# Kernel tuning notes

Measured on AMD Instinct MI355X. Metric: run time of the kernel, lower is better.

Reference implementation:

```python
import jax, jax.numpy as jnp
import numpy as np

N_NODES = 100000
N_EDGES = 1600000
N_CLASS = 26
HIDDEN = 128


def gcn_conv(x, W, b, row, col, ew, n):
    """PyG GCNConv with normalize=True, add_self_loops=True (fill 1.0).

    row/col/ew already include self-loops. x: [N, Fin], W: [Fin, Fout].
    """
    deg = jax.ops.segment_sum(ew, col, num_segments=n)            # [N]
    dis = jnp.where(deg > 0, jax.lax.rsqrt(jnp.maximum(deg, 1e-30)), 0.0)
    norm = dis[row] * ew * dis[col]                               # [E+N]
    h = x @ W                                                     # [N, Fout]
    msg = h[row] * norm[:, None]                                  # gather + scale
    out = jax.ops.segment_sum(msg, col, num_segments=n)           # scatter-add
    return out + b


def setup_inputs() -> dict:
    key = jax.random.key(0)
    k1, k2, k3, k4, k5, k6, k7, k8, k9 = jax.random.split(key, 9)
    x = jax.random.normal(k1, (N_NODES, N_CLASS), dtype=jnp.float32)
    edge_index = jax.random.randint(k2, (2, N_EDGES), 0, N_NODES, dtype=jnp.int64)
    edge_weight = jax.random.uniform(k3, (N_EDGES,), dtype=jnp.float32)
    s1 = 1.0 / np.sqrt(N_CLASS)
    s2 = 1.0 / np.sqrt(HIDDEN)
    W1 = jax.random.uniform(k4, (N_CLASS, HIDDEN), jnp.float32, -s1, s1)
    b1 = jnp.zeros((HIDDEN,), jnp.float32)
    W2 = jax.random.uniform(k5, (HIDDEN, HIDDEN), jnp.float32, -s2, s2)
    b2 = jnp.zeros((HIDDEN,), jnp.float32)
    Wfc = jax.random.uniform(k6, (HIDDEN, N_CLASS), jnp.float32, -s2, s2)
    bfc = jax.random.uniform(k7, (N_CLASS,), jnp.float32, -s2, s2)
    return {"x": x, "edge_index": edge_index, "edge_weight": edge_weight,
            "W1": W1, "b1": b1, "W2": W2, "b2": b2, "Wfc": Wfc, "bfc": bfc}


def reference(x, edge_index, edge_weight, W1, b1, W2, b2, Wfc, bfc):
    n = x.shape[0]
    loop = jnp.arange(n, dtype=edge_index.dtype)
    row = jnp.concatenate([edge_index[0], loop])   # sources (with self-loops)
    col = jnp.concatenate([edge_index[1], loop])   # targets
    ew = jnp.concatenate([edge_weight, jnp.ones((n,), edge_weight.dtype)])
    h = jax.nn.relu(gcn_conv(x, W1, b1, row, col, ew, n))
    h = jax.nn.relu(gcn_conv(h, W2, b2, row, col, ew, n))
    return h @ Wfc + bfc
```

## Files before the change

kernel.cpp:

```cpp
#include <hip/hip_runtime.h>
#include <hip/hip_fp16.h>

#define N_NODES 100000
#define N_EDGES 1600000
#define HIDDEN  128
#define N_CLASS 26

#define BUK_SHIFT 9
#define BUK_DSTS  512
#define NBUK      196
#define BUK_CAP   10240
#define PB_EDGES  8192
#define PB_BLOCKS ((N_EDGES + PB_EDGES - 1) / PB_EDGES)

typedef _Float16 f16x2 __attribute__((ext_vector_type(2)));

__device__ __forceinline__ float fdot2(__half2 a, __half2 b, float c) {
#if __has_builtin(__builtin_amdgcn_fdot2)
    union { __half2 h; f16x2 v; } ua, ub;
    ua.h = a; ub.h = b;
    return __builtin_amdgcn_fdot2(ua.v, ub.v, c, false);
#else
    float2 fa = __half22float2(a), fb = __half22float2(b);
    return c + fa.x * fb.x + fa.y * fb.y;
#endif
}

union U4 { uint4 u; __half2 h[4]; };
union U2 { uint2 u; __half2 h[2]; };
union UW { int i; __half2 h; };


__global__ __launch_bounds__(1024) void bucket_kernel(const int* __restrict__ row,
                                                      const int* __restrict__ col,
                                                      const float* __restrict__ ew,
                                                      int* __restrict__ bukcnt,
                                                      int2* __restrict__ stage) {
    __shared__ int2 outst[PB_EDGES];
    __shared__ unsigned short bukof[PB_EDGES];
    __shared__ int cnt[NBUK], ofs[NBUK], cur[NBUK], gt[NBUK];
    __shared__ int sc[256];
    const int tid = threadIdx.x;
    const int e0 = blockIdx.x * PB_EDGES;
    const int nvalid = min(PB_EDGES, N_EDGES - e0);

    for (int b = tid; b < NBUK; b += 1024) { cnt[b] = 0; cur[b] = 0; }
    __syncthreads();

    int mykey[8]; float myw[8]; int mybuk[8];
#pragma unroll
    for (int i = 0; i < 8; ++i) {
        int idx = tid + i * 1024;
        mybuk[i] = -1;
        if (idx < nvalid) {
            int e = e0 + idx;
            int d = col[e], r = row[e];
            int buk = d >> BUK_SHIFT;
            mykey[i] = ((d & (BUK_DSTS - 1)) << 17) | r;
            myw[i] = ew[e];
            mybuk[i] = buk;
            atomicAdd(&cnt[buk], 1);
        }
    }
    __syncthreads();

    {
        int c = (tid < NBUK) ? cnt[tid] : 0;
        if (tid < 256) sc[tid] = c;
        __syncthreads();
        for (int o = 1; o < 256; o <<= 1) {
            int v = 0;
            if (tid < 256 && tid >= o) v = sc[tid - o];
            __syncthreads();
            if (tid < 256) sc[tid] += v;
            __syncthreads();
        }
        if (tid < NBUK) ofs[tid] = sc[tid] - c;
        __syncthreads();
    }

#pragma unroll
    for (int i = 0; i < 8; ++i) {
        if (mybuk[i] >= 0) {
            int s = ofs[mybuk[i]] + atomicAdd(&cur[mybuk[i]], 1);
            outst[s] = make_int2(mykey[i], __float_as_int(myw[i]));
            bukof[s] = (unsigned short)mybuk[i];
        }
    }
    __syncthreads();

    if (tid < NBUK) {
        int c = cnt[tid];
        int gb = (c > 0) ? atomicAdd(&bukcnt[tid], c) : 0;
        gt[tid] = tid * BUK_CAP + gb;
    }
    __syncthreads();

    for (int i = tid; i < nvalid; i += 1024) {
        int b = bukof[i];
        stage[(size_t)gt[b] + (i - ofs[b])] = outst[i];
    }
}


__global__ void bukscan_kernel(const int* __restrict__ bukcnt, int* __restrict__ bukbase,
                               int* __restrict__ start) {
    __shared__ int s[256];
    int tid = threadIdx.x;
    int c = (tid < NBUK) ? bukcnt[tid] : 0;
    s[tid] = c;
    __syncthreads();
    for (int o = 1; o < 256; o <<= 1) {
        int v = (tid >= o) ? s[tid - o] : 0;
        __syncthreads();
        s[tid] += v;
        __syncthreads();
    }
    if (tid < NBUK) bukbase[tid] = s[tid] - c;
    if (tid == 0) start[N_NODES] = N_EDGES;
}


__global__ __launch_bounds__(1024) void csr_kernel(const int2* __restrict__ stage,
                                                   const int* __restrict__ bukcnt,
                                                   const int* __restrict__ bukbase,
                                                   const float* __restrict__ x,
                                                   int* __restrict__ start,
                                                   float* __restrict__ dinv,
                                                   __half* __restrict__ x16,
                                                   int2* __restrict__ packed,
                                                   int* __restrict__ perm) {
    __shared__ unsigned int cnt5[BUK_DSTS];
    __shared__ int ofs5[BUK_DSTS];
    __shared__ unsigned int cur5[BUK_DSTS];
    __shared__ float deg5[BUK_DSTS];
    __shared__ float dv5[BUK_DSTS];
    __shared__ int sc[BUK_DSTS];
    __shared__ int dhist[128];
    __shared__ int dcur[128];
    const int tid = threadIdx.x;
    const int b = blockIdx.x;
    const int total = bukcnt[b];
    const int base = bukbase[b];
    const int2* st = stage + (size_t)b * BUK_CAP;

    for (int j = tid; j < BUK_DSTS; j += 1024) { cnt5[j] = 0; cur5[j] = 0; deg5[j] = 0.0f; }
    if (tid < 128) { dhist[tid] = 0; dcur[tid] = 0; }
    __syncthreads();

    for (int i = tid; i < total; i += 1024) {
        int2 en = st[i];
        int dl = en.x >> 17;
        atomicAdd(&cnt5[dl], 1u);
        atomicAdd(&deg5[dl], __int_as_float(en.y));
    }
    __syncthreads();

    {
        int c = (tid < BUK_DSTS) ? (int)cnt5[tid] : 0;
        if (tid < BUK_DSTS) sc[tid] = c;
        __syncthreads();
        for (int o = 1; o < BUK_DSTS; o <<= 1) {
            int v = 0;
            if (tid < BUK_DSTS && tid >= o) v = sc[tid - o];
            __syncthreads();
            if (tid < BUK_DSTS) sc[tid] += v;
            __syncthreads();
        }
        if (tid < BUK_DSTS) ofs5[tid] = sc[tid] - c;
        __syncthreads();
    }

    int myd = -1;
    {
        int d = (b << BUK_SHIFT) + tid;
        if (tid < BUK_DSTS && d < N_NODES) {
            myd = min((int)cnt5[tid], 127);
            atomicAdd(&dhist[myd], 1);
        }
    }

    if (tid < BUK_DSTS) {
        int d = (b << BUK_SHIFT) + tid;
        if (d < N_NODES) {
            float dv = rsqrtf(deg5[tid] + 1.0f);
            dv5[tid] = dv;
            dinv[d] = dv;
            start[d] = base + ofs5[tid];
        }
    }
    __syncthreads();

    if (tid < 128) sc[tid] = dhist[tid];
    __syncthreads();
    for (int o = 1; o < 128; o <<= 1) {
        int v = 0;
        if (tid < 128 && tid >= o) v = sc[tid - o];
        __syncthreads();
        if (tid < 128) sc[tid] += v;
        __syncthreads();
    }
    if (myd >= 0) {
        int rank = sc[myd] - dhist[myd] + atomicAdd(&dcur[myd], 1);
        perm[(b << BUK_SHIFT) + rank] = (b << BUK_SHIFT) + tid;
    }

    for (int t = tid; t < BUK_DSTS * 32; t += 1024) {
        int j = t >> 5, l = t & 31;
        int d = (b << BUK_SHIFT) + j;
        if (d < N_NODES) {
            float v = (l < N_CLASS) ? x[(size_t)d * N_CLASS + l] * dv5[j] : 0.0f;
            x16[((size_t)d << 5) + l] = __float2half(v);
        }
    }

    for (int i = tid; i < total; i += 1024) {
        int2 en = st[i];
        int dl = en.x >> 17;
        int src = en.x & 0x1FFFF;
        unsigned int r = atomicAdd(&cur5[dl], 1u);
        unsigned int hw = __half_as_ushort(__float2half(__int_as_float(en.y)));
        packed[(size_t)base + ofs5[dl] + (int)r] = make_int2(src, (int)(hw | (hw << 16)));
    }
}


__global__ __launch_bounds__(256) void layer1_kernel(const __half* __restrict__ x16,
                                                     const int* __restrict__ start,
                                                     const int2* __restrict__ packed,
                                                     const float* __restrict__ dinv,
                                                     const int* __restrict__ perm,
                                                     const float* __restrict__ W1,
                                                     const float* __restrict__ b1,
                                                     __half* __restrict__ h16) {
    __shared__ float axs[32][32];
    __shared__ int gl[32];
    const int tid = threadIdx.x;
    const int nb = blockIdx.x * 32;
    {
        const int j = tid >> 3;
        const int l = tid & 7;
        const int g = perm[nb + j];
        if (l == 0) gl[j] = g;
        const uint2* X = reinterpret_cast<const uint2*>(x16);
        U2 sv; sv.u = X[((size_t)g << 3) + l];
        __half2 acc0 = sv.h[0], acc1 = sv.h[1];
        int s = start[g], t = start[g + 1];
        int i = s;
        for (; i + 8 <= t; i += 8) {
            int2 pk[8]; U2 vv[8];
#pragma unroll
            for (int u = 0; u < 8; ++u) pk[u] = packed[i + u];
#pragma unroll
            for (int u = 0; u < 8; ++u) vv[u].u = X[((size_t)pk[u].x << 3) + l];
#pragma unroll
            for (int u = 0; u < 8; ++u) {
                UW w; w.i = pk[u].y;
                acc0 = __hfma2(w.h, vv[u].h[0], acc0);
                acc1 = __hfma2(w.h, vv[u].h[1], acc1);
            }
        }
        for (; i < t; ++i) {
            int2 p = packed[i];
            U2 v; v.u = X[((size_t)p.x << 3) + l];
            UW w; w.i = p.y;
            acc0 = __hfma2(w.h, v.h[0], acc0); acc1 = __hfma2(w.h, v.h[1], acc1);
        }
        float dg = dinv[g];
        float2 a = __half22float2(acc0), bb = __half22float2(acc1);
        *reinterpret_cast<float4*>(&axs[j][l * 4]) =
            make_float4(dg * a.x, dg * a.y, dg * bb.x, dg * bb.y);
    }
    __syncthreads();
    const int c = tid & 127;
    const int half = tid >> 7;
    float w[N_CLASS];
#pragma unroll
    for (int k = 0; k < N_CLASS; ++k) w[k] = W1[k * HIDDEN + c];
    const float bias = b1[c];
#pragma unroll
    for (int tt = 0; tt < 16; ++tt) {
        int n = half + 2 * tt;
        float acc = bias;
#pragma unroll
        for (int k = 0; k < N_CLASS; ++k) acc += axs[n][k] * w[k];
        h16[(size_t)gl[n] * HIDDEN + c] = __float2half(fmaxf(acc, 0.0f));
    }
}


#define CB_NODES 128
__global__ __launch_bounds__(512) void gemmC_kernel(const __half* __restrict__ h16,
                                                    const float* __restrict__ W2,
                                                    const float* __restrict__ dinv,
                                                    __half* __restrict__ p16) {
    __shared__ __half2 hs2[CB_NODES][HIDDEN / 2];
    __shared__ __half2 ws2[HIDDEN / 2][HIDDEN];
    const int tid = threadIdx.x;
    const int nb = blockIdx.x * CB_NODES;
    for (int t = tid; t < HIDDEN / 2 * HIDDEN; t += 512) {
        int k2 = t >> 7, c = t & 127;
        ws2[k2][c] = __floats2half2_rn(W2[(2 * k2) * HIDDEN + c], W2[(2 * k2 + 1) * HIDDEN + c]);
    }
    for (int t = tid; t < CB_NODES * 16; t += 512) {
        int node = nb + (t >> 4);
        reinterpret_cast<uint4*>(hs2)[t] =
            (node < N_NODES)
                ? reinterpret_cast<const uint4*>(h16)[(size_t)node * 16 + (t & 15)]
                : make_uint4(0u, 0u, 0u, 0u);
    }
    __syncthreads();
    const int c4 = (tid & 31) * 4;
    const int n0 = (tid >> 5) * 8;
    float acc[8][4] = {};
    for (int k2 = 0; k2 < HIDDEN / 2; k2 += 2) {
        U4 wa, wb;
        wa.u = *reinterpret_cast<const uint4*>(&ws2[k2][c4]);
        wb.u = *reinterpret_cast<const uint4*>(&ws2[k2 + 1][c4]);
#pragma unroll
        for (int i = 0; i < 8; ++i) {
            U2 hv; hv.u = *reinterpret_cast<const uint2*>(&hs2[n0 + i][k2]);
#pragma unroll
            for (int q = 0; q < 4; ++q) {
                acc[i][q] = fdot2(hv.h[0], wa.h[q], acc[i][q]);
                acc[i][q] = fdot2(hv.h[1], wb.h[q], acc[i][q]);
            }
        }
    }
#pragma unroll
    for (int i = 0; i < 8; ++i) {
        int node = nb + n0 + i;
        if (node < N_NODES) {
            float d = dinv[node];
            union { __half2 h2[2]; uint2 u; } pk;
            pk.h2[0] = __floats2half2_rn(d * acc[i][0], d * acc[i][1]);
            pk.h2[1] = __floats2half2_rn(d * acc[i][2], d * acc[i][3]);
            *reinterpret_cast<uint2*>(&p16[(size_t)node * HIDDEN + c4]) = pk.u;
        }
    }
}


__global__ __launch_bounds__(256) void agg2_kernel(const __half* __restrict__ p16,
                                                   const int* __restrict__ start,
                                                   const int2* __restrict__ packed,
                                                   const float* __restrict__ dinv,
                                                   const int* __restrict__ perm,
                                                   const float* __restrict__ b2,
                                                   __half* __restrict__ z16) {
    const int grp = threadIdx.x >> 4;
    const int l   = threadIdx.x & 15;
    const int g   = perm[blockIdx.x * 16 + grp];
    const uint4* P = reinterpret_cast<const uint4*>(p16);

    U4 sv; sv.u = P[((size_t)g << 4) + l];
    __half2 acc0 = sv.h[0], acc1 = sv.h[1], acc2 = sv.h[2], acc3 = sv.h[3];

    int s = start[g], t = start[g + 1];
    int i = s;
    for (; i + 8 <= t; i += 8) {
        int2 pk[8]; U4 vv[8];
#pragma unroll
        for (int u = 0; u < 8; ++u) pk[u] = packed[i + u];
#pragma unroll
        for (int u = 0; u < 8; ++u) vv[u].u = P[((size_t)pk[u].x << 4) + l];
#pragma unroll
        for (int u = 0; u < 8; ++u) {
            UW w; w.i = pk[u].y;
            acc0 = __hfma2(w.h, vv[u].h[0], acc0);
            acc1 = __hfma2(w.h, vv[u].h[1], acc1);
            acc2 = __hfma2(w.h, vv[u].h[2], acc2);
            acc3 = __hfma2(w.h, vv[u].h[3], acc3);
        }
    }
    for (; i + 4 <= t; i += 4) {
        int2 pk[4]; U4 vv[4];
#pragma unroll
        for (int u = 0; u < 4; ++u) pk[u] = packed[i + u];
#pragma unroll
        for (int u = 0; u < 4; ++u) vv[u].u = P[((size_t)pk[u].x << 4) + l];
#pragma unroll
        for (int u = 0; u < 4; ++u) {
            UW w; w.i = pk[u].y;
            acc0 = __hfma2(w.h, vv[u].h[0], acc0);
            acc1 = __hfma2(w.h, vv[u].h[1], acc1);
            acc2 = __hfma2(w.h, vv[u].h[2], acc2);
            acc3 = __hfma2(w.h, vv[u].h[3], acc3);
        }
    }
    for (; i < t; ++i) {
        int2 p = packed[i];
        U4 v; v.u = P[((size_t)p.x << 4) + l];
        UW w; w.i = p.y;
        acc0 = __hfma2(w.h, v.h[0], acc0); acc1 = __hfma2(w.h, v.h[1], acc1);
        acc2 = __hfma2(w.h, v.h[2], acc2); acc3 = __hfma2(w.h, v.h[3], acc3);
    }

    const float dg = dinv[g];
    const int f = l * 8;
    float4 ba = *reinterpret_cast<const float4*>(&b2[f]);
    float4 bb = *reinterpret_cast<const float4*>(&b2[f + 4]);
    float2 f0 = __half22float2(acc0), f1 = __half22float2(acc1);
    float2 f2 = __half22float2(acc2), f3 = __half22float2(acc3);
    U4 zz;
    zz.h[0] = __floats2half2_rn(fmaxf(dg * f0.x + ba.x, 0.f), fmaxf(dg * f0.y + ba.y, 0.f));
    zz.h[1] = __floats2half2_rn(fmaxf(dg * f1.x + ba.z, 0.f), fmaxf(dg * f1.y + ba.w, 0.f));
    zz.h[2] = __floats2half2_rn(fmaxf(dg * f2.x + bb.x, 0.f), fmaxf(dg * f2.y + bb.y, 0.f));
    zz.h[3] = __floats2half2_rn(fmaxf(dg * f3.x + bb.z, 0.f), fmaxf(dg * f3.y + bb.w, 0.f));
    reinterpret_cast<uint4*>(z16)[((size_t)g << 4) + l] = zz.u;
}


#define FC_NODES 128
__global__ __launch_bounds__(256) void fc_kernel(const __half* __restrict__ z16,
                                                 const float* __restrict__ Wfc,
                                                 const float* __restrict__ bfc,
                                                 float* __restrict__ out) {
    __shared__ __align__(16) __half2 zsh[FC_NODES][68];
    const int tid = threadIdx.x;
    const int nb = blockIdx.x * FC_NODES;
    for (int t = tid; t < FC_NODES * 16; t += 256) {
        int n = t >> 4, q = t & 15;
        int node = nb + n;
        uint4 v = (node < N_NODES)
                      ? reinterpret_cast<const uint4*>(z16)[(size_t)node * 16 + q]
                      : make_uint4(0u, 0u, 0u, 0u);
        *reinterpret_cast<uint4*>(&zsh[n][q * 4]) = v;
    }
    const int j = tid & 31;
    const int slice = tid >> 5;
    __half2 wreg[HIDDEN / 2];
    float bj = 0.0f;
    if (j < N_CLASS) {
        bj = bfc[j];
#pragma unroll
        for (int k2 = 0; k2 < HIDDEN / 2; ++k2)
            wreg[k2] = __floats2half2_rn(Wfc[(2 * k2) * N_CLASS + j],
                                         Wfc[(2 * k2 + 1) * N_CLASS + j]);
    }
    __syncthreads();
    if (j >= N_CLASS) return;
    for (int n = slice; n < FC_NODES; n += 8) {
        int node = nb + n;
        if (node < N_NODES) {
            float acc = bj;
#pragma unroll
            for (int k2 = 0; k2 < HIDDEN / 2; ++k2)
                acc = fdot2(zsh[n][k2], wreg[k2], acc);
            out[(size_t)node * N_CLASS + j] = acc;
        }
    }
}


extern "C" void kernel_launch(void* const* d_in, const int* in_sizes, int n_in,
                              void* d_out, int out_size, void* d_ws, size_t ws_size,
                              hipStream_t stream) {
    const float* x   = (const float*)d_in[0];
    const int*   ei  = (const int*)  d_in[1];
    const float* ew  = (const float*)d_in[2];
    const float* W1  = (const float*)d_in[3];
    const float* b1  = (const float*)d_in[4];
    const float* W2  = (const float*)d_in[5];
    const float* b2  = (const float*)d_in[6];
    const float* Wfc = (const float*)d_in[7];
    const float* bfc = (const float*)d_in[8];
    float* out = (float*)d_out;

    const int n = N_NODES, E = N_EDGES;
    const int* row = ei;
    const int* col = ei + E;

    char* ws = (char*)d_ws;
    size_t off = 0;
    auto alloc = [&](size_t bytes) -> void* {
        void* ptr = ws + off;
        off += (bytes + 255) & ~(size_t)255;
        return ptr;
    };
    int*   bukcnt  = (int*)  alloc(NBUK * 4);
    int*   bukbase = (int*)  alloc(NBUK * 4);
    float* dinv    = (float*)alloc((size_t)n * 4);
    int*   start   = (int*)  alloc((size_t)(n + 1) * 4);
    int*   perm    = (int*)  alloc((size_t)n * 4);
    int2*  packed  = (int2*) alloc((size_t)E * 8);
    __half* x16    = (__half*)alloc((size_t)n * 32 * 2);
    __half* h16    = (__half*)alloc((size_t)n * HIDDEN * 2 < (size_t)NBUK * BUK_CAP * 8
                                        ? (size_t)NBUK * BUK_CAP * 8
                                        : (size_t)n * HIDDEN * 2);
    __half* p16    = (__half*)alloc((size_t)n * HIDDEN * 2);
    int2*  stage   = (int2*)h16;
    __half* z16    = h16;

    hipMemsetAsync(bukcnt, 0, NBUK * 4, stream);
    bucket_kernel<<<PB_BLOCKS, 1024, 0, stream>>>(row, col, ew, bukcnt, stage);
    bukscan_kernel<<<1, 256, 0, stream>>>(bukcnt, bukbase, start);
    csr_kernel<<<NBUK, 1024, 0, stream>>>(stage, bukcnt, bukbase, x, start, dinv, x16, packed, perm);

    layer1_kernel<<<(n + 31) / 32, 256, 0, stream>>>(x16, start, packed, dinv, perm, W1, b1, h16);

    gemmC_kernel<<<(n + CB_NODES - 1) / CB_NODES, 512, 0, stream>>>(h16, W2, dinv, p16);
    agg2_kernel<<<(n + 15) / 16, 256, 0, stream>>>(p16, start, packed, dinv, perm, b2, z16);

    fc_kernel<<<(n + FC_NODES - 1) / FC_NODES, 256, 0, stream>>>(z16, Wfc, bfc, out);
}
```

Measured before the change: 237.0 us.

## Fuse final linear layer into layer-2 aggregation and use smaller destination buckets

The second-layer aggregation kernel now applies bias and ReLU, stages each node's hidden vector in shared memory, and computes the 26-class output directly from it. This removes the separate fc kernel and the fp16 intermediate write and re-read. Bucketing is also changed to 256 destinations per bucket with 4096 edges per bucket-block, giving about twice as many csr blocks for better GPU occupancy. The costs are redundant per-block staging of Wfc into LDS and an uneven two-pass class loop in which only 10 of 16 lanes work on the second pass. The fused kernel also relies on the 16 lanes of a group sharing a wavefront, since there is no barrier between the shared-memory write and the read.

Result: faster. 224.0 us (-5.5%).

```diff
diff --git a/kernel.cpp b/kernel.cpp
--- a/kernel.cpp
+++ b/kernel.cpp
@@ -6,11 +6,11 @@
 #define HIDDEN  128
 #define N_CLASS 26
 
-#define BUK_SHIFT 9
-#define BUK_DSTS  512
-#define NBUK      196
-#define BUK_CAP   10240
-#define PB_EDGES  8192
+#define BUK_SHIFT 8
+#define BUK_DSTS  256
+#define NBUK      391
+#define BUK_CAP   5120
+#define PB_EDGES  4096
 #define PB_BLOCKS ((N_EDGES + PB_EDGES - 1) / PB_EDGES)
 
 typedef _Float16 f16x2 __attribute__((ext_vector_type(2)));
@@ -31,26 +31,26 @@
 union UW { int i; __half2 h; };
 
 
-__global__ __launch_bounds__(1024) void bucket_kernel(const int* __restrict__ row,
-                                                      const int* __restrict__ col,
-                                                      const float* __restrict__ ew,
-                                                      int* __restrict__ bukcnt,
-                                                      int2* __restrict__ stage) {
+__global__ __launch_bounds__(512) void bucket_kernel(const int* __restrict__ row,
+                                                     const int* __restrict__ col,
+                                                     const float* __restrict__ ew,
+                                                     int* __restrict__ bukcnt,
+                                                     int2* __restrict__ stage) {
     __shared__ int2 outst[PB_EDGES];
     __shared__ unsigned short bukof[PB_EDGES];
     __shared__ int cnt[NBUK], ofs[NBUK], cur[NBUK], gt[NBUK];
-    __shared__ int sc[256];
+    __shared__ int sc[512];
     const int tid = threadIdx.x;
     const int e0 = blockIdx.x * PB_EDGES;
     const int nvalid = min(PB_EDGES, N_EDGES - e0);
 
-    for (int b = tid; b < NBUK; b += 1024) { cnt[b] = 0; cur[b] = 0; }
+    for (int b = tid; b < NBUK; b += 512) { cnt[b] = 0; cur[b] = 0; }
     __syncthreads();
 
     int mykey[8]; float myw[8]; int mybuk[8];
 #pragma unroll
     for (int i = 0; i < 8; ++i) {
-        int idx = tid + i * 1024;
+        int idx = tid + i * 512;
         mybuk[i] = -1;
         if (idx < nvalid) {
             int e = e0 + idx;
@@ -66,13 +66,12 @@
 
     {
         int c = (tid < NBUK) ? cnt[tid] : 0;
-        if (tid < 256) sc[tid] = c;
-        __syncthreads();
-        for (int o = 1; o < 256; o <<= 1) {
-            int v = 0;
-            if (tid < 256 && tid >= o) v = sc[tid - o];
+        sc[tid] = c;
+        __syncthreads();
+        for (int o = 1; o < 512; o <<= 1) {
+            int v = (tid >= o) ? sc[tid - o] : 0;
             __syncthreads();
-            if (tid < 256) sc[tid] += v;
+            sc[tid] += v;
             __syncthreads();
         }
         if (tid < NBUK) ofs[tid] = sc[tid] - c;
@@ -96,7 +95,7 @@
     }
     __syncthreads();
 
-    for (int i = tid; i < nvalid; i += 1024) {
+    for (int i = tid; i < nvalid; i += 512) {
         int b = bukof[i];
         stage[(size_t)gt[b] + (i - ofs[b])] = outst[i];
     }
@@ -105,12 +104,12 @@
 
 __global__ void bukscan_kernel(const int* __restrict__ bukcnt, int* __restrict__ bukbase,
                                int* __restrict__ start) {
-    __shared__ int s[256];
+    __shared__ int s[512];
     int tid = threadIdx.x;
     int c = (tid < NBUK) ? bukcnt[tid] : 0;
     s[tid] = c;
     __syncthreads();
-    for (int o = 1; o < 256; o <<= 1) {
+    for (int o = 1; o < 512; o <<= 1) {
         int v = (tid >= o) ? s[tid - o] : 0;
         __syncthreads();
         s[tid] += v;
@@ -144,7 +143,7 @@
     const int base = bukbase[b];
     const int2* st = stage + (size_t)b * BUK_CAP;
 
-    for (int j = tid; j < BUK_DSTS; j += 1024) { cnt5[j] = 0; cur5[j] = 0; deg5[j] = 0.0f; }
+    if (tid < BUK_DSTS) { cnt5[tid] = 0; cur5[tid] = 0; deg5[tid] = 0.0f; }
     if (tid < 128) { dhist[tid] = 0; dcur[tid] = 0; }
     __syncthreads();
 
@@ -341,15 +340,28 @@
 }
 
 
-__global__ __launch_bounds__(256) void agg2_kernel(const __half* __restrict__ p16,
-                                                   const int* __restrict__ start,
-                                                   const int2* __restrict__ packed,
-                                                   const float* __restrict__ dinv,
-                                                   const int* __restrict__ perm,
-                                                   const float* __restrict__ b2,
-                                                   __half* __restrict__ z16) {
-    const int grp = threadIdx.x >> 4;
-    const int l   = threadIdx.x & 15;
+__global__ __launch_bounds__(256) void aggfc_kernel(const __half* __restrict__ p16,
+                                                    const int* __restrict__ start,
+                                                    const int2* __restrict__ packed,
+                                                    const float* __restrict__ dinv,
+                                                    const int* __restrict__ perm,
+                                                    const float* __restrict__ b2,
+                                                    const float* __restrict__ Wfc,
+                                                    const float* __restrict__ bfc,
+                                                    float* __restrict__ out) {
+    __shared__ __half2 wf2[HIDDEN / 2][N_CLASS];
+    __shared__ float bfs[N_CLASS];
+    __shared__ __half2 zs2[16][65];
+    const int tid = threadIdx.x;
+    for (int t = tid; t < HIDDEN / 2 * N_CLASS; t += 256) {
+        int k2 = t / N_CLASS, j = t % N_CLASS;
+        wf2[k2][j] = __floats2half2_rn(Wfc[(2 * k2) * N_CLASS + j], Wfc[(2 * k2 + 1) * N_CLASS + j]);
+    }
+    if (tid < N_CLASS) bfs[tid] = bfc[tid];
+    __syncthreads();
+
+    const int grp = tid >> 4;
+    const int l   = tid & 15;
     const int g   = perm[blockIdx.x * 16 + grp];
     const uint4* P = reinterpret_cast<const uint4*>(p16);
 
@@ -402,53 +414,17 @@
     float4 bb = *reinterpret_cast<const float4*>(&b2[f + 4]);
     float2 f0 = __half22float2(acc0), f1 = __half22float2(acc1);
     float2 f2 = __half22float2(acc2), f3 = __half22float2(acc3);
-    U4 zz;
-    zz.h[0] = __floats2half2_rn(fmaxf(dg * f0.x + ba.x, 0.f), fmaxf(dg * f0.y + ba.y, 0.f));
-    zz.h[1] = __floats2half2_rn(fmaxf(dg * f1.x + ba.z, 0.f), fmaxf(dg * f1.y + ba.w, 0.f));
-    zz.h[2] = __floats2half2_rn(fmaxf(dg * f2.x + bb.x, 0.f), fmaxf(dg * f2.y + bb.y, 0.f));
-    zz.h[3] = __floats2half2_rn(fmaxf(dg * f3.x + bb.z, 0.f), fmaxf(dg * f3.y + bb.w, 0.f));
-    reinterpret_cast<uint4*>(z16)[((size_t)g << 4) + l] = zz.u;
-}
-
-
-#define FC_NODES 128
-__global__ __launch_bounds__(256) void fc_kernel(const __half* __restrict__ z16,
-                                                 const float* __restrict__ Wfc,
-                                                 const float* __restrict__ bfc,
-                                                 float* __restrict__ out) {
-    __shared__ __align__(16) __half2 zsh[FC_NODES][68];
-    const int tid = threadIdx.x;
-    const int nb = blockIdx.x * FC_NODES;
-    for (int t = tid; t < FC_NODES * 16; t += 256) {
-        int n = t >> 4, q = t & 15;
-        int node = nb + n;
-        uint4 v = (node < N_NODES)
-                      ? reinterpret_cast<const uint4*>(z16)[(size_t)node * 16 + q]
-                      : make_uint4(0u, 0u, 0u, 0u);
-        *reinterpret_cast<uint4*>(&zsh[n][q * 4]) = v;
-    }
-    const int j = tid & 31;
-    const int slice = tid >> 5;
-    __half2 wreg[HIDDEN / 2];
-    float bj = 0.0f;
-    if (j < N_CLASS) {
-        bj = bfc[j];
-#pragma unroll
+    zs2[grp][l * 4 + 0] = __floats2half2_rn(fmaxf(dg * f0.x + ba.x, 0.f), fmaxf(dg * f0.y + ba.y, 0.f));
+    zs2[grp][l * 4 + 1] = __floats2half2_rn(fmaxf(dg * f1.x + ba.z, 0.f), fmaxf(dg * f1.y + ba.w, 0.f));
+    zs2[grp][l * 4 + 2] = __floats2half2_rn(fmaxf(dg * f2.x + bb.x, 0.f), fmaxf(dg * f2.y + bb.y, 0.f));
+    zs2[grp][l * 4 + 3] = __floats2half2_rn(fmaxf(dg * f3.x + bb.z, 0.f), fmaxf(dg * f3.y + bb.w, 0.f));
+#pragma unroll
+    for (int jj = l; jj < N_CLASS; jj += 16) {
+        float accf = bfs[jj];
+#pragma unroll 16
         for (int k2 = 0; k2 < HIDDEN / 2; ++k2)
-            wreg[k2] = __floats2half2_rn(Wfc[(2 * k2) * N_CLASS + j],
-                                         Wfc[(2 * k2 + 1) * N_CLASS + j]);
-    }
-    __syncthreads();
-    if (j >= N_CLASS) return;
-    for (int n = slice; n < FC_NODES; n += 8) {
-        int node = nb + n;
-        if (node < N_NODES) {
-            float acc = bj;
-#pragma unroll
-            for (int k2 = 0; k2 < HIDDEN / 2; ++k2)
-                acc = fdot2(zsh[n][k2], wreg[k2], acc);
-            out[(size_t)node * N_CLASS + j] = acc;
-        }
+            accf = fdot2(zs2[grp][k2], wf2[k2][jj], accf);
+        out[(size_t)g * N_CLASS + jj] = accf;
     }
 }
 
@@ -490,17 +466,14 @@
                                         : (size_t)n * HIDDEN * 2);
     __half* p16    = (__half*)alloc((size_t)n * HIDDEN * 2);
     int2*  stage   = (int2*)h16;
-    __half* z16    = h16;
 
     hipMemsetAsync(bukcnt, 0, NBUK * 4, stream);
-    bucket_kernel<<<PB_BLOCKS, 1024, 0, stream>>>(row, col, ew, bukcnt, stage);
-    bukscan_kernel<<<1, 256, 0, stream>>>(bukcnt, bukbase, start);
+    bucket_kernel<<<PB_BLOCKS, 512, 0, stream>>>(row, col, ew, bukcnt, stage);
+    bukscan_kernel<<<1, 512, 0, stream>>>(bukcnt, bukbase, start);
     csr_kernel<<<NBUK, 1024, 0, stream>>>(stage, bukcnt, bukbase, x, start, dinv, x16, packed, perm);
 
     layer1_kernel<<<(n + 31) / 32, 256, 0, stream>>>(x16, start, packed, dinv, perm, W1, b1, h16);
 
     gemmC_kernel<<<(n + CB_NODES - 1) / CB_NODES, 512, 0, stream>>>(h16, W2, dinv, p16);
-    agg2_kernel<<<(n + 15) / 16, 256, 0, stream>>>(p16, start, packed, dinv, perm, b2, z16);
-
-    fc_kernel<<<(n + FC_NODES - 1) / FC_NODES, 256, 0, stream>>>(z16, Wfc, bfc, out);
-}
+    aggfc_kernel<<<(n + 15) / 16, 256, 0, stream>>>(p16, start, packed, dinv, perm, b2, Wfc, bfc, out);
+}
```
